# Kernel tuning notes

Hardware: AMD Instinct MI355X
Metric: run time of the kernel (lower is better)

The kernel has to match this reference:

```python
import jax, jax.numpy as jnp
import numpy as np

B, T, C, HEAD_SIZE = 512, 128, 1024, 128
BLOCK_SIZE = 128  # module's registered tril buffer size


def setup_inputs() -> dict:
    key = jax.random.key(0)
    k0, k1, k2, k3 = jax.random.split(key, 4)
    idx = jax.random.normal(k0, (B, T, C), dtype=jnp.float32)
    # torch Linear(note_dimensions, head_size, bias=False); stored here as [in, out]
    Wk = jax.random.normal(k1, (C, HEAD_SIZE), dtype=jnp.float32) * 0.02
    Wq = jax.random.normal(k2, (C, HEAD_SIZE), dtype=jnp.float32) * 0.02
    Wv = jax.random.normal(k3, (C, HEAD_SIZE), dtype=jnp.float32) * 0.02
    return {"idx": idx, "Wk": Wk, "Wq": Wq, "Wv": Wv}


def reference(idx, Wk, Wq, Wv):
    # q, k, v: [B, T, H]
    k = idx @ Wk
    q = idx @ Wq
    v = idx @ Wv
    # NOTE: original multiplies by head_size**0.5 (not divides) - kept faithful.
    weights = jnp.einsum('bth,bsh->bts', q, k) * (HEAD_SIZE ** 0.5)  # [B, T, T]
    causal = jnp.tril(jnp.ones((T, T), dtype=bool))
    weights = jnp.where(causal, weights, -jnp.inf)
    # NOTE: original applies softmax over dim=1 (query axis) - kept faithful.
    activations = jax.nn.softmax(weights, axis=1)
    # dropout is identity in eval/reference mode
    out = jnp.einsum('bts,bsh->bth', activations, v)  # [B, T, H]
    return out
```

## Files before the change

### kernel.cpp

```cpp
#include <hip/hip_runtime.h>
#include <hip/hip_bf16.h>


typedef __attribute__((ext_vector_type(8))) __bf16 bf16x8;
typedef __attribute__((ext_vector_type(4))) float f32x4;
typedef __attribute__((ext_vector_type(4))) unsigned short u16x4;
typedef __attribute__((ext_vector_type(8))) unsigned short u16x8;

#define SQRT_H 11.313708498984761f

__device__ __forceinline__ void splitf(float a, unsigned short& hi, unsigned short& lo) {
    unsigned u = __float_as_uint(a);
    hi = (unsigned short)(u >> 16);
    float r = a - __uint_as_float(u & 0xFFFF0000u);
    lo = (unsigned short)(__float_as_uint(r) >> 16);
}

__global__ __launch_bounds__(256) void prep_w(
    const float* __restrict__ Wq, const float* __restrict__ Wk, const float* __restrict__ Wv,
    unsigned short* __restrict__ W2hi, unsigned short* __restrict__ W2lo)
{
    __shared__ __align__(16) unsigned short thi[128][128];
    __shared__ __align__(16) unsigned short tlo[128][128];
    const float* W = (blockIdx.y == 0) ? Wq : (blockIdx.y == 1 ? Wk : Wv);
    const int c0 = blockIdx.x * 128;
    const int tid = threadIdx.x;
    #pragma unroll
    for (int it = 0; it < 16; ++it) {
        int chunk = tid + it * 256;
        int cl = chunk >> 5, f4 = chunk & 31;
        float4 v = *(const float4*)(W + (size_t)(c0 + cl) * 128 + f4 * 4);
        unsigned short h, l;
        splitf(v.x, h, l); thi[cl][f4*4+0] = h; tlo[cl][f4*4+0] = l;
        splitf(v.y, h, l); thi[cl][f4*4+1] = h; tlo[cl][f4*4+1] = l;
        splitf(v.z, h, l); thi[cl][f4*4+2] = h; tlo[cl][f4*4+2] = l;
        splitf(v.w, h, l); thi[cl][f4*4+3] = h; tlo[cl][f4*4+3] = l;
    }
    __syncthreads();
    #pragma unroll
    for (int it = 0; it < 8; ++it) {
        int chunk = tid + it * 256;
        int h = chunk >> 4, slot = chunk & 15;
        u16x8 vh, vl;
        #pragma unroll
        for (int e = 0; e < 8; ++e) { vh[e] = thi[slot*8+e][h]; vl[e] = tlo[slot*8+e][h]; }
        size_t off = (size_t)(blockIdx.y * 128 + h) * 1024 + c0 + slot * 8;
        *(u16x8*)(W2hi + off) = vh;
        *(u16x8*)(W2lo + off) = vl;
    }
}

__global__ __launch_bounds__(256, 2) void qkv_gemm(
    const float* __restrict__ idx,
    const unsigned short* __restrict__ W2hi, const unsigned short* __restrict__ W2lo,
    float* __restrict__ qo, float* __restrict__ ko, float* __restrict__ vT)
{
    __shared__ __align__(16) char smem[65536];
    const int tid  = threadIdx.x;
    const int lane = tid & 63;
    const int wid  = tid >> 6;
    const int wr = wid >> 1, wc = wid & 1;
    const int l16 = lane & 15, lgr = lane >> 4;
    const int hw = blockIdx.x;
    const int logical = (hw & 7) * 192 + (hw >> 3);
    const int mt = logical / 3;
    const int nt = logical - mt * 3;

    f32x4 acc[4][4];
    #pragma unroll
    for (int m = 0; m < 4; ++m)
        #pragma unroll
        for (int n = 0; n < 4; ++n) acc[m][n] = (f32x4){0.f, 0.f, 0.f, 0.f};

    const float* Ag = idx + (size_t)mt * (128 * 1024);
    const unsigned short* Bhg = W2hi + (size_t)nt * 128 * 1024;
    const unsigned short* Blg = W2lo + (size_t)nt * 128 * 1024;

    for (int ks = 0; ks < 1024; ks += 64) {
        __syncthreads();
        #pragma unroll
        for (int it = 0; it < 8; ++it) {
            int chunk = tid + it * 256;
            int row = chunk >> 4, f4 = chunk & 15;
            float4 v = *(const float4*)(Ag + (size_t)row * 1024 + ks + f4 * 4);
            unsigned short h0,h1,h2,h3,l0,l1,l2,l3;
            splitf(v.x,h0,l0); splitf(v.y,h1,l1); splitf(v.z,h2,l2); splitf(v.w,h3,l3);
            u16x4 hv = {h0,h1,h2,h3}, lv = {l0,l1,l2,l3};
            int off = row * 128 + ((f4 * 8) ^ ((row & 7) << 4));
            *(u16x4*)(smem + off)         = hv;
            *(u16x4*)(smem + 16384 + off) = lv;
        }
        #pragma unroll
        for (int it = 0; it < 4; ++it) {
            int chunk = tid + it * 256;
            int row = chunk >> 3, slot = chunk & 7;
            size_t goff = (size_t)row * 1024 + ks + slot * 8;
            u16x8 bh = *(const u16x8*)(Bhg + goff);
            u16x8 bl = *(const u16x8*)(Blg + goff);
            int off = row * 128 + ((slot * 16) ^ ((row & 7) << 4));
            *(u16x8*)(smem + 32768 + off) = bh;
            *(u16x8*)(smem + 49152 + off) = bl;
        }
        __syncthreads();
        #pragma unroll
        for (int kk = 0; kk < 64; kk += 32) {
            const int kbyte = (kk + lgr * 8) * 2;
            bf16x8 ahi[4], alo[4], bhi[4], blo[4];
            #pragma unroll
            for (int m = 0; m < 4; ++m) {
                int row = wr * 64 + m * 16 + l16;
                int off = row * 128 + (kbyte ^ ((row & 7) << 4));
                ahi[m] = *(const bf16x8*)(smem + off);
                alo[m] = *(const bf16x8*)(smem + 16384 + off);
            }
            #pragma unroll
            for (int n = 0; n < 4; ++n) {
                int row = wc * 64 + n * 16 + l16;
                int off = row * 128 + (kbyte ^ ((row & 7) << 4));
                bhi[n] = *(const bf16x8*)(smem + 32768 + off);
                blo[n] = *(const bf16x8*)(smem + 49152 + off);
            }
            #pragma unroll
            for (int m = 0; m < 4; ++m)
                #pragma unroll
                for (int n = 0; n < 4; ++n) {
                    acc[m][n] = __builtin_amdgcn_mfma_f32_16x16x32_bf16(ahi[m], bhi[n], acc[m][n], 0, 0, 0);
                    acc[m][n] = __builtin_amdgcn_mfma_f32_16x16x32_bf16(alo[m], bhi[n], acc[m][n], 0, 0, 0);
                    acc[m][n] = __builtin_amdgcn_mfma_f32_16x16x32_bf16(ahi[m], blo[n], acc[m][n], 0, 0, 0);
                }
        }
    }
    if (nt == 2) {
        float* outp = vT + (size_t)mt * (128 * 128);
        #pragma unroll
        for (int m = 0; m < 4; ++m)
            #pragma unroll
            for (int n = 0; n < 4; ++n) {
                int t = wr * 64 + m * 16 + lgr * 4;
                int h = wc * 64 + n * 16 + l16;
                *(f32x4*)(outp + (size_t)h * 128 + t) = acc[m][n];
            }
    } else {
        float* outp = (nt == 0 ? qo : ko) + (size_t)mt * (128 * 128);
        #pragma unroll
        for (int m = 0; m < 4; ++m)
            #pragma unroll
            for (int n = 0; n < 4; ++n)
                #pragma unroll
                for (int j = 0; j < 4; ++j) {
                    int t = wr * 64 + m * 16 + lgr * 4 + j;
                    int h = wc * 64 + n * 16 + l16;
                    outp[(size_t)t * 128 + h] = acc[m][n][j];
                }
    }
}

__global__ __launch_bounds__(512, 4) void attn(
    const float* __restrict__ qg, const float* __restrict__ kg,
    const float* __restrict__ vTg, float* __restrict__ outg)
{
    __shared__ __align__(16) char smem[67584];
    float* scrM = (float*)(smem + 65536);
    float* scrS = (float*)(smem + 66560);

    const int tid  = threadIdx.x;
    const int lane = tid & 63;
    const int wid  = tid >> 6;
    const int wr = wid >> 2, wc = wid & 3;
    const int l16 = lane & 15, lgr = lane >> 4;
    const int b = blockIdx.x;

    const float* qb = qg  + (size_t)b * 16384;
    const float* kb = kg  + (size_t)b * 16384;
    const float* vb = vTg + (size_t)b * 16384;

    #pragma unroll
    for (int it = 0; it < 8; ++it) {
        int chunk = tid + it * 512;
        int row = chunk >> 5, f4 = chunk & 31;
        float4 vk = *(const float4*)(kb + (size_t)row * 128 + f4 * 4);
        unsigned short h0,h1,h2,h3,l0,l1,l2,l3;
        splitf(vk.x,h0,l0); splitf(vk.y,h1,l1); splitf(vk.z,h2,l2); splitf(vk.w,h3,l3);
        int off = row * 256 + ((f4 * 8) ^ ((row & 7) << 4));
        *(u16x4*)(smem + off)         = (u16x4){h0,h1,h2,h3};
        *(u16x4*)(smem + 32768 + off) = (u16x4){l0,l1,l2,l3};
    }
    __syncthreads();

    f32x4 accs[4][2];
    #pragma unroll
    for (int m = 0; m < 4; ++m) { accs[m][0] = (f32x4){0.f,0.f,0.f,0.f}; accs[m][1] = (f32x4){0.f,0.f,0.f,0.f}; }
    #pragma unroll
    for (int kk = 0; kk < 128; kk += 32) {
        const int kbyte = (kk + lgr * 8) * 2;
        bf16x8 kh[2], kl[2];
        #pragma unroll
        for (int n = 0; n < 2; ++n) {
            int row = wc * 32 + n * 16 + l16;
            int off = row * 256 + (kbyte ^ ((row & 7) << 4));
            kh[n] = *(const bf16x8*)(smem + off);
            kl[n] = *(const bf16x8*)(smem + 32768 + off);
        }
        #pragma unroll
        for (int m = 0; m < 4; ++m) {
            int trow = wr * 64 + m * 16 + l16;
            float4 a0 = *(const float4*)(qb + trow * 128 + kk + lgr * 8);
            float4 a1 = *(const float4*)(qb + trow * 128 + kk + lgr * 8 + 4);
            unsigned short hh[8], ll[8];
            splitf(a0.x,hh[0],ll[0]); splitf(a0.y,hh[1],ll[1]);
            splitf(a0.z,hh[2],ll[2]); splitf(a0.w,hh[3],ll[3]);
            splitf(a1.x,hh[4],ll[4]); splitf(a1.y,hh[5],ll[5]);
            splitf(a1.z,hh[6],ll[6]); splitf(a1.w,hh[7],ll[7]);
            u16x8 qh8 = {hh[0],hh[1],hh[2],hh[3],hh[4],hh[5],hh[6],hh[7]};
            u16x8 ql8 = {ll[0],ll[1],ll[2],ll[3],ll[4],ll[5],ll[6],ll[7]};
            bf16x8 qh = *(bf16x8*)&qh8, ql = *(bf16x8*)&ql8;
            #pragma unroll
            for (int n = 0; n < 2; ++n) {
                accs[m][n] = __builtin_amdgcn_mfma_f32_16x16x32_bf16(qh, kh[n], accs[m][n], 0, 0, 0);
                accs[m][n] = __builtin_amdgcn_mfma_f32_16x16x32_bf16(ql, kh[n], accs[m][n], 0, 0, 0);
                accs[m][n] = __builtin_amdgcn_mfma_f32_16x16x32_bf16(qh, kl[n], accs[m][n], 0, 0, 0);
            }
        }
    }
    __syncthreads();

    float cmax[2] = {-3e38f, -3e38f};
    #pragma unroll
    for (int m = 0; m < 4; ++m)
        #pragma unroll
        for (int n = 0; n < 2; ++n)
            #pragma unroll
            for (int j = 0; j < 4; ++j) {
                int t = wr * 64 + m * 16 + lgr * 4 + j;
                int s = wc * 32 + n * 16 + l16;
                float val = accs[m][n][j] * SQRT_H;
                val = (t >= s) ? val : -1e30f;
                accs[m][n][j] = val;
                cmax[n] = fmaxf(cmax[n], val);
            }
    #pragma unroll
    for (int n = 0; n < 2; ++n) {
        cmax[n] = fmaxf(cmax[n], __shfl_xor(cmax[n], 16));
        cmax[n] = fmaxf(cmax[n], __shfl_xor(cmax[n], 32));
    }
    if (lgr == 0) {
        scrM[(wr * 4 + wc) * 32 + l16]      = cmax[0];
        scrM[(wr * 4 + wc) * 32 + 16 + l16] = cmax[1];
    }
    __syncthreads();
    float mm[2];
    #pragma unroll
    for (int n = 0; n < 2; ++n)
        mm[n] = fmaxf(scrM[wc * 32 + n * 16 + l16], scrM[(4 + wc) * 32 + n * 16 + l16]);

    float csum[2] = {0.f, 0.f};
    #pragma unroll
    for (int m = 0; m < 4; ++m)
        #pragma unroll
        for (int n = 0; n < 2; ++n)
            #pragma unroll
            for (int j = 0; j < 4; ++j) {
                float e = __expf(accs[m][n][j] - mm[n]);
                accs[m][n][j] = e;
                csum[n] += e;
            }
    #pragma unroll
    for (int n = 0; n < 2; ++n) {
        csum[n] += __shfl_xor(csum[n], 16);
        csum[n] += __shfl_xor(csum[n], 32);
    }
    if (lgr == 0) {
        scrS[(wr * 4 + wc) * 32 + l16]      = csum[0];
        scrS[(wr * 4 + wc) * 32 + 16 + l16] = csum[1];
    }
    __syncthreads();
    float inv[2];
    #pragma unroll
    for (int n = 0; n < 2; ++n)
        inv[n] = 1.f / (scrS[wc * 32 + n * 16 + l16] + scrS[(4 + wc) * 32 + n * 16 + l16]);

    #pragma unroll
    for (int m = 0; m < 4; ++m)
        #pragma unroll
        for (int n = 0; n < 2; ++n)
            #pragma unroll
            for (int j = 0; j < 4; ++j) {
                int t = wr * 64 + m * 16 + lgr * 4 + j;
                int s = wc * 32 + n * 16 + l16;
                float a = accs[m][n][j] * inv[n];
                unsigned short hi, lo; splitf(a, hi, lo);
                int off = t * 256 + ((s * 2) ^ ((t & 7) << 4));
                *(unsigned short*)(smem + off)         = hi;
                *(unsigned short*)(smem + 32768 + off) = lo;
            }
    __syncthreads();

    f32x4 acco[4][2];
    #pragma unroll
    for (int m = 0; m < 4; ++m) { acco[m][0] = (f32x4){0.f,0.f,0.f,0.f}; acco[m][1] = (f32x4){0.f,0.f,0.f,0.f}; }
    #pragma unroll
    for (int kk = 0; kk < 128; kk += 32) {
        const int kbyte = (kk + lgr * 8) * 2;
        bf16x8 vh[2], vl[2];
        #pragma unroll
        for (int n = 0; n < 2; ++n) {
            int hrow = wc * 32 + n * 16 + l16;
            float4 v0 = *(const float4*)(vb + hrow * 128 + kk + lgr * 8);
            float4 v1 = *(const float4*)(vb + hrow * 128 + kk + lgr * 8 + 4);
            unsigned short hh[8], ll[8];
            splitf(v0.x,hh[0],ll[0]); splitf(v0.y,hh[1],ll[1]);
            splitf(v0.z,hh[2],ll[2]); splitf(v0.w,hh[3],ll[3]);
            splitf(v1.x,hh[4],ll[4]); splitf(v1.y,hh[5],ll[5]);
            splitf(v1.z,hh[6],ll[6]); splitf(v1.w,hh[7],ll[7]);
            u16x8 vh8 = {hh[0],hh[1],hh[2],hh[3],hh[4],hh[5],hh[6],hh[7]};
            u16x8 vl8 = {ll[0],ll[1],ll[2],ll[3],ll[4],ll[5],ll[6],ll[7]};
            vh[n] = *(bf16x8*)&vh8; vl[n] = *(bf16x8*)&vl8;
        }
        #pragma unroll
        for (int m = 0; m < 4; ++m) {
            int arow = wr * 64 + m * 16 + l16;
            int off = arow * 256 + (kbyte ^ ((arow & 7) << 4));
            bf16x8 ah = *(const bf16x8*)(smem + off);
            bf16x8 al = *(const bf16x8*)(smem + 32768 + off);
            #pragma unroll
            for (int n = 0; n < 2; ++n) {
                acco[m][n] = __builtin_amdgcn_mfma_f32_16x16x32_bf16(ah, vh[n], acco[m][n], 0, 0, 0);
                acco[m][n] = __builtin_amdgcn_mfma_f32_16x16x32_bf16(al, vh[n], acco[m][n], 0, 0, 0);
                acco[m][n] = __builtin_amdgcn_mfma_f32_16x16x32_bf16(ah, vl[n], acco[m][n], 0, 0, 0);
            }
        }
    }
    float* ob = outg + (size_t)b * 16384;
    #pragma unroll
    for (int m = 0; m < 4; ++m)
        #pragma unroll
        for (int n = 0; n < 2; ++n)
            #pragma unroll
            for (int j = 0; j < 4; ++j) {
                int t = wr * 64 + m * 16 + lgr * 4 + j;
                int h = wc * 32 + n * 16 + l16;
                ob[(size_t)t * 128 + h] = acco[m][n][j];
            }
}

extern "C" void kernel_launch(void* const* d_in, const int* in_sizes, int n_in,
                              void* d_out, int out_size, void* d_ws, size_t ws_size,
                              hipStream_t stream) {
    const float* idx = (const float*)d_in[0];
    const float* Wk  = (const float*)d_in[1];
    const float* Wq  = (const float*)d_in[2];
    const float* Wv  = (const float*)d_in[3];
    float* out = (float*)d_out;

    char* ws = (char*)d_ws;
    float* qb = (float*)(ws);
    float* kb = (float*)(ws + 33554432);
    float* vT = (float*)(ws + 67108864);
    unsigned short* W2hi = (unsigned short*)(ws + 100663296);
    unsigned short* W2lo = (unsigned short*)(ws + 101449728);

    prep_w<<<dim3(8, 3), 256, 0, stream>>>(Wq, Wk, Wv, W2hi, W2lo);
    qkv_gemm<<<dim3(512 * 3), 256, 0, stream>>>(idx, W2hi, W2lo, qb, kb, vT);
    attn<<<dim3(512), 512, 0, stream>>>(qb, kb, vT, out);
}
```

Before: 499.7 us.

## Fuse QKV projections per batch tile and drop low-order bf16 terms for V

```diff
diff --git a/kernel.cpp b/kernel.cpp
--- a/kernel.cpp
+++ b/kernel.cpp
@@ -6,6 +6,7 @@
 typedef __attribute__((ext_vector_type(4))) float f32x4;
 typedef __attribute__((ext_vector_type(4))) unsigned short u16x4;
 typedef __attribute__((ext_vector_type(8))) unsigned short u16x8;
+typedef __attribute__((ext_vector_type(4))) unsigned int u32x4;
 
 #define SQRT_H 11.313708498984761f
 
@@ -14,6 +15,11 @@
     hi = (unsigned short)(u >> 16);
     float r = a - __uint_as_float(u & 0xFFFF0000u);
     lo = (unsigned short)(__float_as_uint(r) >> 16);
+}
+
+__device__ __forceinline__ unsigned short bf16rne(float a) {
+    unsigned u = __float_as_uint(a);
+    return (unsigned short)((u + 0x7fffu + ((u >> 16) & 1u)) >> 16);
 }
 
 __global__ __launch_bounds__(256) void prep_w(
@@ -50,62 +56,59 @@
     }
 }
 
-__global__ __launch_bounds__(256, 2) void qkv_gemm(
+__global__ __launch_bounds__(512, 2) void qkv_fused(
     const float* __restrict__ idx,
     const unsigned short* __restrict__ W2hi, const unsigned short* __restrict__ W2lo,
-    float* __restrict__ qo, float* __restrict__ ko, float* __restrict__ vT)
+    unsigned int* __restrict__ qpk, unsigned int* __restrict__ kpk,
+    unsigned short* __restrict__ vT)
 {
-    __shared__ __align__(16) char smem[65536];
+    __shared__ __align__(16) char smem[114688];
     const int tid  = threadIdx.x;
     const int lane = tid & 63;
     const int wid  = tid >> 6;
-    const int wr = wid >> 1, wc = wid & 1;
+    const int wr = wid >> 2, wc = wid & 3;
     const int l16 = lane & 15, lgr = lane >> 4;
-    const int hw = blockIdx.x;
-    const int logical = (hw & 7) * 192 + (hw >> 3);
-    const int mt = logical / 3;
-    const int nt = logical - mt * 3;
-
-    f32x4 acc[4][4];
-    #pragma unroll
-    for (int m = 0; m < 4; ++m)
-        #pragma unroll
-        for (int n = 0; n < 4; ++n) acc[m][n] = (f32x4){0.f, 0.f, 0.f, 0.f};
+    const int mt = blockIdx.x;
+
+    f32x4 acc[4][6];
+    #pragma unroll
+    for (int m = 0; m < 4; ++m)
+        #pragma unroll
+        for (int n = 0; n < 6; ++n) acc[m][n] = (f32x4){0.f, 0.f, 0.f, 0.f};
 
     const float* Ag = idx + (size_t)mt * (128 * 1024);
-    const unsigned short* Bhg = W2hi + (size_t)nt * 128 * 1024;
-    const unsigned short* Blg = W2lo + (size_t)nt * 128 * 1024;
 
     for (int ks = 0; ks < 1024; ks += 64) {
         __syncthreads();
         #pragma unroll
-        for (int it = 0; it < 8; ++it) {
-            int chunk = tid + it * 256;
+        for (int it = 0; it < 4; ++it) {
+            int chunk = tid + it * 512;
             int row = chunk >> 4, f4 = chunk & 15;
             float4 v = *(const float4*)(Ag + (size_t)row * 1024 + ks + f4 * 4);
             unsigned short h0,h1,h2,h3,l0,l1,l2,l3;
             splitf(v.x,h0,l0); splitf(v.y,h1,l1); splitf(v.z,h2,l2); splitf(v.w,h3,l3);
-            u16x4 hv = {h0,h1,h2,h3}, lv = {l0,l1,l2,l3};
             int off = row * 128 + ((f4 * 8) ^ ((row & 7) << 4));
-            *(u16x4*)(smem + off)         = hv;
-            *(u16x4*)(smem + 16384 + off) = lv;
-        }
-        #pragma unroll
-        for (int it = 0; it < 4; ++it) {
-            int chunk = tid + it * 256;
-            int row = chunk >> 3, slot = chunk & 7;
-            size_t goff = (size_t)row * 1024 + ks + slot * 8;
-            u16x8 bh = *(const u16x8*)(Bhg + goff);
-            u16x8 bl = *(const u16x8*)(Blg + goff);
-            int off = row * 128 + ((slot * 16) ^ ((row & 7) << 4));
+            *(u16x4*)(smem + off)         = (u16x4){h0,h1,h2,h3};
+            *(u16x4*)(smem + 16384 + off) = (u16x4){l0,l1,l2,l3};
+        }
+        #pragma unroll
+        for (int it = 0; it < 6; ++it) {
+            int chunk = tid + it * 512;
+            int r = chunk >> 3, slot = chunk & 7;
+            size_t goff = (size_t)r * 1024 + ks + slot * 8;
+            u16x8 bh = *(const u16x8*)(W2hi + goff);
+            int off = r * 128 + ((slot * 16) ^ ((r & 7) << 4));
             *(u16x8*)(smem + 32768 + off) = bh;
-            *(u16x8*)(smem + 49152 + off) = bl;
+            if (r < 256) {
+                u16x8 bl = *(const u16x8*)(W2lo + goff);
+                *(u16x8*)(smem + 81920 + off) = bl;
+            }
         }
         __syncthreads();
         #pragma unroll
         for (int kk = 0; kk < 64; kk += 32) {
             const int kbyte = (kk + lgr * 8) * 2;
-            bf16x8 ahi[4], alo[4], bhi[4], blo[4];
+            bf16x8 ahi[4], alo[4];
             #pragma unroll
             for (int m = 0; m < 4; ++m) {
                 int row = wr * 64 + m * 16 + l16;
@@ -114,54 +117,56 @@
                 alo[m] = *(const bf16x8*)(smem + 16384 + off);
             }
             #pragma unroll
-            for (int n = 0; n < 4; ++n) {
-                int row = wc * 64 + n * 16 + l16;
-                int off = row * 128 + (kbyte ^ ((row & 7) << 4));
-                bhi[n] = *(const bf16x8*)(smem + 32768 + off);
-                blo[n] = *(const bf16x8*)(smem + 49152 + off);
-            }
-            #pragma unroll
-            for (int m = 0; m < 4; ++m)
+            for (int n = 0; n < 6; ++n) {
+                int brow = n * 64 + wc * 16 + l16;
+                int boff = brow * 128 + (kbyte ^ ((brow & 7) << 4));
+                bf16x8 bh = *(const bf16x8*)(smem + 32768 + boff);
+                if (n < 4) {
+                    bf16x8 bl = *(const bf16x8*)(smem + 81920 + boff);
+                    #pragma unroll
+                    for (int m = 0; m < 4; ++m) {
+                        acc[m][n] = __builtin_amdgcn_mfma_f32_16x16x32_bf16(ahi[m], bh, acc[m][n], 0, 0, 0);
+                        acc[m][n] = __builtin_amdgcn_mfma_f32_16x16x32_bf16(alo[m], bh, acc[m][n], 0, 0, 0);
+                        acc[m][n] = __builtin_amdgcn_mfma_f32_16x16x32_bf16(ahi[m], bl, acc[m][n], 0, 0, 0);
+                    }
+                } else {
+                    #pragma unroll
+                    for (int m = 0; m < 4; ++m)
+                        acc[m][n] = __builtin_amdgcn_mfma_f32_16x16x32_bf16(ahi[m], bh, acc[m][n], 0, 0, 0);
+                }
+            }
+        }
+    }
+    #pragma unroll
+    for (int m = 0; m < 4; ++m)
+        #pragma unroll
+        for (int n = 0; n < 6; ++n) {
+            const int p = n >> 1;
+            const int h = (n & 1) * 64 + wc * 16 + l16;
+            const int t0 = wr * 64 + m * 16 + lgr * 4;
+            if (p == 2) {
+                u16x4 vv;
                 #pragma unroll
-                for (int n = 0; n < 4; ++n) {
-                    acc[m][n] = __builtin_amdgcn_mfma_f32_16x16x32_bf16(ahi[m], bhi[n], acc[m][n], 0, 0, 0);
-                    acc[m][n] = __builtin_amdgcn_mfma_f32_16x16x32_bf16(alo[m], bhi[n], acc[m][n], 0, 0, 0);
-                    acc[m][n] = __builtin_amdgcn_mfma_f32_16x16x32_bf16(ahi[m], blo[n], acc[m][n], 0, 0, 0);
-                }
-        }
-    }
-    if (nt == 2) {
-        float* outp = vT + (size_t)mt * (128 * 128);
-        #pragma unroll
-        for (int m = 0; m < 4; ++m)
-            #pragma unroll
-            for (int n = 0; n < 4; ++n) {
-                int t = wr * 64 + m * 16 + lgr * 4;
-                int h = wc * 64 + n * 16 + l16;
-                *(f32x4*)(outp + (size_t)h * 128 + t) = acc[m][n];
-            }
-    } else {
-        float* outp = (nt == 0 ? qo : ko) + (size_t)mt * (128 * 128);
-        #pragma unroll
-        for (int m = 0; m < 4; ++m)
-            #pragma unroll
-            for (int n = 0; n < 4; ++n)
+                for (int j = 0; j < 4; ++j) vv[j] = bf16rne(acc[m][n][j]);
+                *(u16x4*)(vT + (size_t)mt * 16384 + (size_t)h * 128 + t0) = vv;
+            } else {
+                unsigned int* dst = (p == 0 ? qpk : kpk) + (size_t)mt * 16384;
                 #pragma unroll
                 for (int j = 0; j < 4; ++j) {
-                    int t = wr * 64 + m * 16 + lgr * 4 + j;
-                    int h = wc * 64 + n * 16 + l16;
-                    outp[(size_t)t * 128 + h] = acc[m][n][j];
+                    unsigned short hi, lo; splitf(acc[m][n][j], hi, lo);
+                    dst[(size_t)(t0 + j) * 128 + h] = (unsigned)hi | ((unsigned)lo << 16);
                 }
-    }
+            }
+        }
 }
 
 __global__ __launch_bounds__(512, 4) void attn(
-    const float* __restrict__ qg, const float* __restrict__ kg,
-    const float* __restrict__ vTg, float* __restrict__ outg)
+    const unsigned int* __restrict__ qpk, const unsigned int* __restrict__ kpk,
+    const unsigned short* __restrict__ vTg, float* __restrict__ outg)
 {
-    __shared__ __align__(16) char smem[67584];
-    float* scrM = (float*)(smem + 65536);
-    float* scrS = (float*)(smem + 66560);
+    __shared__ __align__(16) char smem[34816];
+    float* scrM = (float*)(smem + 32768);
+    float* scrS = (float*)(smem + 33792);
 
     const int tid  = threadIdx.x;
     const int lane = tid & 63;
@@ -170,50 +175,42 @@
     const int l16 = lane & 15, lgr = lane >> 4;
     const int b = blockIdx.x;
 
-    const float* qb = qg  + (size_t)b * 16384;
-    const float* kb = kg  + (size_t)b * 16384;
-    const float* vb = vTg + (size_t)b * 16384;
-
-    #pragma unroll
-    for (int it = 0; it < 8; ++it) {
-        int chunk = tid + it * 512;
-        int row = chunk >> 5, f4 = chunk & 31;
-        float4 vk = *(const float4*)(kb + (size_t)row * 128 + f4 * 4);
-        unsigned short h0,h1,h2,h3,l0,l1,l2,l3;
-        splitf(vk.x,h0,l0); splitf(vk.y,h1,l1); splitf(vk.z,h2,l2); splitf(vk.w,h3,l3);
-        int off = row * 256 + ((f4 * 8) ^ ((row & 7) << 4));
-        *(u16x4*)(smem + off)         = (u16x4){h0,h1,h2,h3};
-        *(u16x4*)(smem + 32768 + off) = (u16x4){l0,l1,l2,l3};
-    }
-    __syncthreads();
+    const unsigned int*   qb = qpk + (size_t)b * 16384;
+    const unsigned int*   kb = kpk + (size_t)b * 16384;
+    const unsigned short* vb = vTg + (size_t)b * 16384;
 
     f32x4 accs[4][2];
     #pragma unroll
     for (int m = 0; m < 4; ++m) { accs[m][0] = (f32x4){0.f,0.f,0.f,0.f}; accs[m][1] = (f32x4){0.f,0.f,0.f,0.f}; }
     #pragma unroll
     for (int kk = 0; kk < 128; kk += 32) {
-        const int kbyte = (kk + lgr * 8) * 2;
+        const int h0 = kk + lgr * 8;
         bf16x8 kh[2], kl[2];
         #pragma unroll
         for (int n = 0; n < 2; ++n) {
-            int row = wc * 32 + n * 16 + l16;
-            int off = row * 256 + (kbyte ^ ((row & 7) << 4));
-            kh[n] = *(const bf16x8*)(smem + off);
-            kl[n] = *(const bf16x8*)(smem + 32768 + off);
+            int srow = wc * 32 + n * 16 + l16;
+            const unsigned int* kp = kb + srow * 128 + h0;
+            u32x4 p0 = *(const u32x4*)kp, p1 = *(const u32x4*)(kp + 4);
+            u16x8 hh, ll;
+            #pragma unroll
+            for (int e = 0; e < 4; ++e) {
+                hh[e] = (unsigned short)p0[e];  ll[e] = (unsigned short)(p0[e] >> 16);
+                hh[4+e] = (unsigned short)p1[e]; ll[4+e] = (unsigned short)(p1[e] >> 16);
+            }
+            kh[n] = *(bf16x8*)&hh; kl[n] = *(bf16x8*)&ll;
         }
         #pragma unroll
         for (int m = 0; m < 4; ++m) {
             int trow = wr * 64 + m * 16 + l16;
-            float4 a0 = *(const float4*)(qb + trow * 128 + kk + lgr * 8);
-            float4 a1 = *(const float4*)(qb + trow * 128 + kk + lgr * 8 + 4);
-            unsigned short hh[8], ll[8];
-            splitf(a0.x,hh[0],ll[0]); splitf(a0.y,hh[1],ll[1]);
-            splitf(a0.z,hh[2],ll[2]); splitf(a0.w,hh[3],ll[3]);
-            splitf(a1.x,hh[4],ll[4]); splitf(a1.y,hh[5],ll[5]);
-            splitf(a1.z,hh[6],ll[6]); splitf(a1.w,hh[7],ll[7]);
-            u16x8 qh8 = {hh[0],hh[1],hh[2],hh[3],hh[4],hh[5],hh[6],hh[7]};
-            u16x8 ql8 = {ll[0],ll[1],ll[2],ll[3],ll[4],ll[5],ll[6],ll[7]};
-            bf16x8 qh = *(bf16x8*)&qh8, ql = *(bf16x8*)&ql8;
+            const unsigned int* qp = qb + trow * 128 + h0;
+            u32x4 p0 = *(const u32x4*)qp, p1 = *(const u32x4*)(qp + 4);
+            u16x8 hh, ll;
+            #pragma unroll
+            for (int e = 0; e < 4; ++e) {
+                hh[e] = (unsigned short)p0[e];  ll[e] = (unsigned short)(p0[e] >> 16);
+                hh[4+e] = (unsigned short)p1[e]; ll[4+e] = (unsigned short)(p1[e] >> 16);
+            }
+            bf16x8 qh = *(bf16x8*)&hh, ql = *(bf16x8*)&ll;
             #pragma unroll
             for (int n = 0; n < 2; ++n) {
                 accs[m][n] = __builtin_amdgcn_mfma_f32_16x16x32_bf16(qh, kh[n], accs[m][n], 0, 0, 0);
@@ -222,7 +219,6 @@
             }
         }
     }
-    __syncthreads();
 
     float cmax[2] = {-3e38f, -3e38f};
     #pragma unroll
@@ -287,11 +283,9 @@
             for (int j = 0; j < 4; ++j) {
                 int t = wr * 64 + m * 16 + lgr * 4 + j;
                 int s = wc * 32 + n * 16 + l16;
-                float a = accs[m][n][j] * inv[n];
-                unsigned short hi, lo; splitf(a, hi, lo);
+                unsigned short a = bf16rne(accs[m][n][j] * inv[n]);
                 int off = t * 256 + ((s * 2) ^ ((t & 7) << 4));
-                *(unsigned short*)(smem + off)         = hi;
-                *(unsigned short*)(smem + 32768 + off) = lo;
+                *(unsigned short*)(smem + off) = a;
             }
     __syncthreads();
 
@@ -300,34 +294,21 @@
     for (int m = 0; m < 4; ++m) { acco[m][0] = (f32x4){0.f,0.f,0.f,0.f}; acco[m][1] = (f32x4){0.f,0.f,0.f,0.f}; }
     #pragma unroll
     for (int kk = 0; kk < 128; kk += 32) {
-        const int kbyte = (kk + lgr * 8) * 2;
-        bf16x8 vh[2], vl[2];
+        const int s0 = kk + lgr * 8;
+        bf16x8 vh[2];
         #pragma unroll
         for (int n = 0; n < 2; ++n) {
             int hrow = wc * 32 + n * 16 + l16;
-            float4 v0 = *(const float4*)(vb + hrow * 128 + kk + lgr * 8);
-            float4 v1 = *(const float4*)(vb + hrow * 128 + kk + lgr * 8 + 4);
-            unsigned short hh[8], ll[8];
-            splitf(v0.x,hh[0],ll[0]); splitf(v0.y,hh[1],ll[1]);
-            splitf(v0.z,hh[2],ll[2]); splitf(v0.w,hh[3],ll[3]);
-            splitf(v1.x,hh[4],ll[4]); splitf(v1.y,hh[5],ll[5]);
-            splitf(v1.z,hh[6],ll[6]); splitf(v1.w,hh[7],ll[7]);
-            u16x8 vh8 = {hh[0],hh[1],hh[2],hh[3],hh[4],hh[5],hh[6],hh[7]};
-            u16x8 vl8 = {ll[0],ll[1],ll[2],ll[3],ll[4],ll[5],ll[6],ll[7]};
-            vh[n] = *(bf16x8*)&vh8; vl[n] = *(bf16x8*)&vl8;
+            vh[n] = *(const bf16x8*)(vb + hrow * 128 + s0);
         }
         #pragma unroll
         for (int m = 0; m < 4; ++m) {
             int arow = wr * 64 + m * 16 + l16;
-            int off = arow * 256 + (kbyte ^ ((arow & 7) << 4));
+            int off = arow * 256 + ((s0 * 2) ^ ((arow & 7) << 4));
             bf16x8 ah = *(const bf16x8*)(smem + off);
-            bf16x8 al = *(const bf16x8*)(smem + 32768 + off);
-            #pragma unroll
-            for (int n = 0; n < 2; ++n) {
+            #pragma unroll
+            for (int n = 0; n < 2; ++n)
                 acco[m][n] = __builtin_amdgcn_mfma_f32_16x16x32_bf16(ah, vh[n], acco[m][n], 0, 0, 0);
-                acco[m][n] = __builtin_amdgcn_mfma_f32_16x16x32_bf16(al, vh[n], acco[m][n], 0, 0, 0);
-                acco[m][n] = __builtin_amdgcn_mfma_f32_16x16x32_bf16(ah, vl[n], acco[m][n], 0, 0, 0);
-            }
         }
     }
     float* ob = outg + (size_t)b * 16384;
@@ -353,13 +334,13 @@
     float* out = (float*)d_out;
 
     char* ws = (char*)d_ws;
-    float* qb = (float*)(ws);
-    float* kb = (float*)(ws + 33554432);
-    float* vT = (float*)(ws + 67108864);
-    unsigned short* W2hi = (unsigned short*)(ws + 100663296);
-    unsigned short* W2lo = (unsigned short*)(ws + 101449728);
+    unsigned int*   qpk  = (unsigned int*)(ws);
+    unsigned int*   kpk  = (unsigned int*)(ws + 33554432);
+    unsigned short* vT   = (unsigned short*)(ws + 67108864);
+    unsigned short* W2hi = (unsigned short*)(ws + 83886080);
+    unsigned short* W2lo = (unsigned short*)(ws + 84672512);
 
     prep_w<<<dim3(8, 3), 256, 0, stream>>>(Wq, Wk, Wv, W2hi, W2lo);
-    qkv_gemm<<<dim3(512 * 3), 256, 0, stream>>>(idx, W2hi, W2lo, qb, kb, vT);
-    attn<<<dim3(512), 512, 0, stream>>>(qb, kb, vT, out);
-}
+    qkv_fused<<<dim3(512), 512, 0, stream>>>(idx, W2hi, W2lo, qpk, kpk, vT);
+    attn<<<dim3(512), 512, 0, stream>>>(qpk, kpk, vT, out);
+}
```

Measured after the change: 495.6 us. About the same (-0.8%).
